# Optimization experiments

Measured on AMD Instinct MI355X. Metric: run time of the kernel, lower is better.

## Reference

```python
import jax, jax.numpy as jnp
import numpy as np

N_DOMAINS = 8
LN_EPS = 1e-5


def setup_inputs() -> dict:
    key = jax.random.key(0)
    ks = jax.random.split(key, 4)
    N, D_IN, D_HID, D_OUT = 32768, 256, 1024, 256
    x = jax.random.normal(ks[0], (N, D_IN), dtype=jnp.float32)
    domain_types = jax.random.randint(ks[1], (N,), 0, N_DOMAINS, dtype=jnp.int32)
    # Per-domain MLP parameters (8 independent experts)
    W1 = jax.random.normal(ks[2], (N_DOMAINS, D_IN, D_HID), dtype=jnp.float32) * (1.0 / np.sqrt(D_IN))
    b1 = jnp.zeros((N_DOMAINS, D_HID), dtype=jnp.float32)
    gamma = jnp.ones((N_DOMAINS, D_HID), dtype=jnp.float32)
    beta = jnp.zeros((N_DOMAINS, D_HID), dtype=jnp.float32)
    W2 = jax.random.normal(ks[3], (N_DOMAINS, D_HID, D_OUT), dtype=jnp.float32) * (1.0 / np.sqrt(D_HID))
    b2 = jnp.zeros((N_DOMAINS, D_OUT), dtype=jnp.float32)
    return {"x": x, "domain_types": domain_types, "W1": W1, "b1": b1,
            "gamma": gamma, "beta": beta, "W2": W2, "b2": b2}


def _expert_mlp(x, W1d, b1d, gd, bd, W2d, b2d):
    # Linear -> LayerNorm -> ReLU -> (Dropout: identity at eval) -> Linear
    h = x @ W1d + b1d                       # [N, hid]
    mu = jnp.mean(h, axis=-1, keepdims=True)
    var = jnp.mean(jnp.square(h - mu), axis=-1, keepdims=True)
    h = (h - mu) * jax.lax.rsqrt(var + LN_EPS) * gd + bd
    h = jax.nn.relu(h)
    return h @ W2d + b2d                    # [N, out]


def reference(x, domain_types, W1, b1, gamma, beta, W2, b2):
    # output dim == x.shape[-1] (as in the torch code: zeros(batch, x.shape[-1]))
    out = jnp.zeros((x.shape[0], x.shape[-1]), dtype=x.dtype)
    for d in range(N_DOMAINS):  # small fixed expert loop (static MoE dispatch)
        y = _expert_mlp(x, W1[d], b1[d], gamma[d], beta[d], W2[d], b2[d])
        mask = (domain_types == d)[:, None]
        out = jnp.where(mask, y, out)
    return out
```

## Files before the change

kernel.cpp:

```cpp
#include <hip/hip_runtime.h>
#include <hip/hip_bf16.h>


#define ND 8
#define NROWS 32768
#define DIN 256
#define DHID 1024
#define DOUT 256
#define MPAD 33792
#define NTILES 264

typedef short short8 __attribute__((ext_vector_type(8)));
typedef float floatx4 __attribute__((ext_vector_type(4)));

__device__ __forceinline__ unsigned short f2bf(float f) {
    unsigned u = __builtin_bit_cast(unsigned, f);
    unsigned r = u + 0x7fff + ((u >> 16) & 1);
    return (unsigned short)(r >> 16);
}
__device__ __forceinline__ float bf2f(unsigned short h) {
    unsigned u = ((unsigned)h) << 16;
    return __builtin_bit_cast(float, u);
}

#define GLDS16(gp, lp) __builtin_amdgcn_global_load_lds( \
    (const __attribute__((address_space(1))) void*)(gp), \
    (__attribute__((address_space(3))) void*)(lp), 16, 0, 0)

__global__ void transpose_both(const float* __restrict__ W1, unsigned short* __restrict__ W1T,
                               const float* __restrict__ W2, unsigned short* __restrict__ W2T,
                               int* __restrict__ cnt) {
    if (blockIdx.x == 0 && threadIdx.x < 16) cnt[threadIdx.x] = 0;
    __shared__ float t[32][33];
    int b = blockIdx.x;
    const float* in; unsigned short* out; int R, C, bx, by, z;
    if (b < 2048) {
        in = W1; out = W1T; R = DIN; C = DHID;
        bx = b & 31; by = (b >> 5) & 7; z = b >> 8;
    } else {
        b -= 2048;
        in = W2; out = W2T; R = DHID; C = DOUT;
        bx = b & 7; by = (b >> 3) & 31; z = b >> 8;
    }
    const int c0 = bx * 32, r0 = by * 32;
    const int tx = threadIdx.x & 31, ty = threadIdx.x >> 5;
    const float* src = in + (size_t)z * R * C;
    unsigned short* dst = out + (size_t)z * R * C;
#pragma unroll
    for (int i = 0; i < 32; i += 8)
        t[ty + i][tx] = src[(size_t)(r0 + ty + i) * C + c0 + tx];
    __syncthreads();
#pragma unroll
    for (int i = 0; i < 32; i += 8)
        dst[(size_t)(c0 + ty + i) * R + r0 + tx] = f2bf(t[tx][ty + i]);
}

__global__ void init_histo(const int* __restrict__ dt, int* __restrict__ perm,
                           int* __restrict__ counts) {
    const int i = blockIdx.x * 256 + threadIdx.x;
    if (i < MPAD) perm[i] = -1;
    __shared__ int lc[ND];
    if (threadIdx.x < ND) lc[threadIdx.x] = 0;
    __syncthreads();
    if (i < NROWS) atomicAdd(&lc[dt[i]], 1);
    __syncthreads();
    if (threadIdx.x < ND && lc[threadIdx.x] > 0)
        atomicAdd(&counts[threadIdx.x], lc[threadIdx.x]);
}

__global__ void make_meta(const int* __restrict__ counts, int* __restrict__ cursors,
                          int2* __restrict__ meta) {
    __shared__ int base[ND], ntc[ND];
    const int t = threadIdx.x;
    if (t == 0) {
        int off = 0;
        for (int d = 0; d < ND; d++) {
            base[d] = off;
            ntc[d] = (counts[d] + 127) >> 7;
            cursors[d] = off;
            off += ntc[d] << 7;
        }
    }
    __syncthreads();
    for (int i = t; i < NTILES; i += 64) {
        int2 m = make_int2(-1, 0);
#pragma unroll
        for (int d = 0; d < ND; d++) {
            const int ti = i - (base[d] >> 7);
            if (ti >= 0 && ti < ntc[d]) m = make_int2(d, base[d] + (ti << 7));
        }
        meta[i] = m;
    }
}

__global__ __launch_bounds__(256)
void assign_pos(const int* __restrict__ dt, int* __restrict__ cursors,
                int* __restrict__ perm, int* __restrict__ pos) {
    __shared__ int lcnt[ND];
    __shared__ int lbase[ND];
    const int tid = threadIdx.x;
    if (tid < ND) lcnt[tid] = 0;
    __syncthreads();
    const int r = blockIdx.x * 256 + tid;
    const int d = dt[r];
    const int myrank = atomicAdd(&lcnt[d], 1);
    __syncthreads();
    if (tid < ND && lcnt[tid] > 0)
        lbase[tid] = atomicAdd(&cursors[tid], lcnt[tid]);
    __syncthreads();
    const int p = lbase[d] + myrank;
    pos[r] = p;
    perm[p] = r;
}

__global__ __launch_bounds__(256)
void copy_rows(const float* __restrict__ x, const int* __restrict__ pos,
               unsigned short* __restrict__ xs) {
    const int tid = threadIdx.x;
    const int lane = tid & 63;
    const int r = blockIdx.x * 4 + (tid >> 6);
    const int p = pos[r];
    float4 v = ((const float4*)(x + (size_t)r * DIN))[lane];
    ushort4 o;
    o.x = f2bf(v.x); o.y = f2bf(v.y); o.z = f2bf(v.z); o.w = f2bf(v.w);
    ((ushort4*)(xs + (size_t)p * DIN))[lane] = o;
}

template <int K, bool ISB>
__global__ __launch_bounds__(256, 2)
void gemm_bt(const unsigned short* __restrict__ A,
             const unsigned short* __restrict__ Bt,
             const float* __restrict__ bias,
             const int2* __restrict__ meta,
             const int* __restrict__ perm,
             unsigned short* __restrict__ Cbf,
             float* __restrict__ Cf,
             const int Ntot,
             float2* __restrict__ spart,
             const float* __restrict__ gamma,
             const float* __restrict__ beta) {
    constexpr int NB = ISB ? 2 : 8;
    constexpr int NWG = NTILES * NB;
    constexpr int NS = K / 32;
    const int bid = (int)blockIdx.x;
    const int wid = (bid & 7) * (NWG >> 3) + (bid >> 3);
    const int tile = wid / NB;
    const int n0 = (wid % NB) * 128;
    const int2 md = meta[tile];
    const int dom = md.x;
    if (dom < 0) return;
    const int m0 = md.y;

    __shared__ unsigned short As[2][128 * 32];
    __shared__ unsigned short Bs[2][128 * 32];
    __shared__ float gb[ISB ? 2048 : 64];
    __shared__ float sred[2][128];

    const int tid = threadIdx.x;
    const int lane = tid & 63;
    const int w = tid >> 6;
    const int wr = w >> 1, wc = w & 1;
    const int l15 = lane & 15;

    const unsigned short* Abase = A + (size_t)m0 * K;
    const unsigned short* Bbase = Bt + (size_t)dom * Ntot * K + (size_t)n0 * K;

    if (!ISB) {
        if (tid < 128) { sred[0][tid] = 0.f; sred[1][tid] = 0.f; }
    }

    const int ma = (w * 128 + lane) >> 2;
    const int kc = lane & 3;
    float muv[2], rsv[2];
    short8 hv0{}, hv1{};
    if (ISB) {
        ((float4*)gb)[tid] = ((const float4*)(gamma + dom * DHID))[tid];
        ((float4*)(gb + 1024))[tid] = ((const float4*)(beta + dom * DHID))[tid];
#pragma unroll
        for (int h2 = 0; h2 < 2; ++h2) {
            const int rm = m0 + ma + h2 * 16;
            float s = 0.f, s2 = 0.f;
#pragma unroll
            for (int nb = 0; nb < 8; ++nb) {
                const float2 p = spart[(size_t)nb * MPAD + rm];
                s += p.x; s2 += p.y;
            }
            const float mu = s * (1.f / 1024.f);
            const float var = fmaxf(s2 * (1.f / 1024.f) - mu * mu, 0.f);
            muv[h2] = mu;
            rsv[h2] = rsqrtf(var + 1e-5f);
        }
        hv0 = *(const short8*)(Abase + (size_t)ma * K + kc * 8);
        hv1 = *(const short8*)(Abase + (size_t)(ma + 16) * K + kc * 8);
    }

#define STAGE_B(buf, t_) {                                                     \
        const int k0_ = (t_) * 32;                                             \
        _Pragma("unroll")                                                      \
        for (int it = 0; it < 2; ++it) {                                       \
            const int c = w * 128 + it * 64 + lane;                            \
            const int m_ = c >> 2, kcc = c & 3;                                \
            GLDS16(Bbase + (size_t)m_ * K + k0_ + kcc * 8,                     \
                   &Bs[buf][(w * 128 + it * 64) * 8]);                         \
        }                                                                      \
    }
#define STAGE_A_GLDS(buf, t_) {                                                \
        const int k0_ = (t_) * 32;                                             \
        _Pragma("unroll")                                                      \
        for (int it = 0; it < 2; ++it) {                                       \
            const int c = w * 128 + it * 64 + lane;                            \
            const int m_ = c >> 2, kcc = c & 3;                                \
            GLDS16(Abase + (size_t)m_ * K + k0_ + kcc * 8,                     \
                   &As[buf][(w * 128 + it * 64) * 8]);                         \
        }                                                                      \
    }
#define STAGE_A_XFRM(buf, t_) {                                                \
        const int k1 = (t_) * 32 + kc * 8;                                     \
        const float4 g0 = *(const float4*)&gb[k1];                             \
        const float4 g1 = *(const float4*)&gb[k1 + 4];                         \
        const float4 e0 = *(const float4*)&gb[1024 + k1];                      \
        const float4 e1 = *(const float4*)&gb[1024 + k1 + 4];                  \
        const float gA[8] = {g0.x, g0.y, g0.z, g0.w, g1.x, g1.y, g1.z, g1.w};  \
        const float eA[8] = {e0.x, e0.y, e0.z, e0.w, e1.x, e1.y, e1.z, e1.w};  \
        _Pragma("unroll")                                                      \
        for (int h2 = 0; h2 < 2; ++h2) {                                       \
            const float mu = muv[h2], rs = rsv[h2];                            \
            const short8 hvv = h2 ? hv1 : hv0;                                 \
            short8 o;                                                          \
            _Pragma("unroll")                                                  \
            for (int e = 0; e < 8; ++e) {                                      \
                const float rg = gA[e] * rs;                                   \
                const float v = fmaxf(fmaf(bf2f((unsigned short)hvv[e]), rg,   \
                                           fmaf(-mu, rg, eA[e])), 0.f);        \
                o[e] = (short)f2bf(v);                                         \
            }                                                                  \
            *(short8*)&As[buf][(w * 128 + h2 * 64 + lane) * 8] = o;            \
        }                                                                      \
    }
#define LOAD_H(t_) {                                                           \
        const int k0_ = (t_) * 32;                                             \
        hv0 = *(const short8*)(Abase + (size_t)ma * K + k0_ + kc * 8);         \
        hv1 = *(const short8*)(Abase + (size_t)(ma + 16) * K + k0_ + kc * 8);  \
    }

    floatx4 acc[4][4];
#pragma unroll
    for (int i = 0; i < 4; i++)
#pragma unroll
        for (int j = 0; j < 4; j++) acc[i][j] = 0.f;

    STAGE_B(0, 0)
    if (!ISB) {
        STAGE_A_GLDS(0, 0)
    } else {
        STAGE_A_XFRM(0, 0)
        LOAD_H(1)
    }
    __syncthreads();

    int cur = 0;
    const int kk = (lane >> 4) * 8;
    for (int t = 0; t < NS - 1; ++t) {
        const int nx = cur ^ 1;
        STAGE_B(nx, t + 1)
        if (!ISB) {
            STAGE_A_GLDS(nx, t + 1)
        } else {
            STAGE_A_XFRM(nx, t + 1)
            if (t + 2 < NS) LOAD_H(t + 2)
        }
        short8 a[4], b[4];
#pragma unroll
        for (int i = 0; i < 4; i++) {
            const int m = wr * 64 + i * 16 + l15;
            a[i] = *(const short8*)&As[cur][m * 32 + kk];
            const int n = wc * 64 + i * 16 + l15;
            b[i] = *(const short8*)&Bs[cur][n * 32 + kk];
        }
        __builtin_amdgcn_s_setprio(1);
#pragma unroll
        for (int i = 0; i < 4; i++)
#pragma unroll
            for (int j = 0; j < 4; j++)
                acc[i][j] = __builtin_amdgcn_mfma_f32_16x16x32_bf16(a[i], b[j], acc[i][j], 0, 0, 0);
        __builtin_amdgcn_s_setprio(0);
        __syncthreads();
        cur = nx;
    }
    {
        short8 a[4], b[4];
#pragma unroll
        for (int i = 0; i < 4; i++) {
            const int m = wr * 64 + i * 16 + l15;
            a[i] = *(const short8*)&As[cur][m * 32 + kk];
            const int n = wc * 64 + i * 16 + l15;
            b[i] = *(const short8*)&Bs[cur][n * 32 + kk];
        }
        __builtin_amdgcn_s_setprio(1);
#pragma unroll
        for (int i = 0; i < 4; i++)
#pragma unroll
            for (int j = 0; j < 4; j++)
                acc[i][j] = __builtin_amdgcn_mfma_f32_16x16x32_bf16(a[i], b[j], acc[i][j], 0, 0, 0);
        __builtin_amdgcn_s_setprio(0);
    }
#undef STAGE_B
#undef STAGE_A_GLDS
#undef STAGE_A_XFRM
#undef LOAD_H

    const int quad = lane >> 4;
    if (!ISB) {
        float bv[4];
#pragma unroll
        for (int j = 0; j < 4; j++)
            bv[j] = bias[dom * Ntot + n0 + wc * 64 + j * 16 + l15];
#pragma unroll
        for (int i = 0; i < 4; i++) {
#pragma unroll
            for (int r = 0; r < 4; r++) {
                const int rl = wr * 64 + i * 16 + quad * 4 + r;
                float s = 0.f, s2 = 0.f;
#pragma unroll
                for (int j = 0; j < 4; j++) {
                    const float v = acc[i][j][r] + bv[j];
                    Cbf[(size_t)(m0 + rl) * Ntot + n0 + wc * 64 + j * 16 + l15] = f2bf(v);
                    s += v; s2 += v * v;
                }
#pragma unroll
                for (int o = 8; o; o >>= 1) {
                    s  += __shfl_xor(s, o, 64);
                    s2 += __shfl_xor(s2, o, 64);
                }
                if (l15 == 0) {
                    atomicAdd(&sred[0][rl], s);
                    atomicAdd(&sred[1][rl], s2);
                }
            }
        }
        __syncthreads();
        if (tid < 128)
            spart[(size_t)(n0 >> 7) * MPAD + m0 + tid] =
                make_float2(sred[0][tid], sred[1][tid]);
    } else {
#pragma unroll
        for (int i = 0; i < 4; i++) {
            const int rowbase = m0 + wr * 64 + i * 16 + quad * 4;
#pragma unroll
            for (int r = 0; r < 4; r++) {
                const int orig = perm[rowbase + r];
                if (orig < 0) continue;
#pragma unroll
                for (int j = 0; j < 4; j++) {
                    const int col = n0 + wc * 64 + j * 16 + l15;
                    Cf[(size_t)orig * Ntot + col] = acc[i][j][r] + bias[dom * Ntot + col];
                }
            }
        }
    }
}

extern "C" void kernel_launch(void* const* d_in, const int* in_sizes, int n_in,
                              void* d_out, int out_size, void* d_ws, size_t ws_size,
                              hipStream_t stream) {
    const float* x = (const float*)d_in[0];
    const int* dt = (const int*)d_in[1];
    const float* W1 = (const float*)d_in[2];
    const float* b1 = (const float*)d_in[3];
    const float* gamma = (const float*)d_in[4];
    const float* beta = (const float*)d_in[5];
    const float* W2 = (const float*)d_in[6];
    const float* b2 = (const float*)d_in[7];
    float* out = (float*)d_out;

    char* ws = (char*)d_ws;
    size_t off = 0;
    auto take = [&](size_t nbytes) -> char* {
        char* p = ws + off;
        off = (off + nbytes + 255) & ~(size_t)255;
        return p;
    };
    unsigned short* W1T = (unsigned short*)take((size_t)ND * DHID * DIN * 2);
    unsigned short* W2T = (unsigned short*)take((size_t)ND * DOUT * DHID * 2);
    unsigned short* XS  = (unsigned short*)take((size_t)MPAD * DIN * 2);
    unsigned short* H   = (unsigned short*)take((size_t)MPAD * DHID * 2);
    float2* SPART = (float2*)take((size_t)8 * MPAD * 8);
    int* PERM   = (int*)take(MPAD * 4);
    int* POS    = (int*)take(NROWS * 4);
    int* CNT    = (int*)take(64);
    int2* META  = (int2*)take(NTILES * 8);
    (void)ws_size; (void)n_in; (void)in_sizes; (void)out_size;

    int* COUNTS = CNT;
    int* CURSORS = CNT + 8;

    transpose_both<<<4096, 256, 0, stream>>>(W1, W1T, W2, W2T, CNT);
    init_histo<<<MPAD / 256, 256, 0, stream>>>(dt, PERM, COUNTS);
    make_meta<<<1, 64, 0, stream>>>(COUNTS, CURSORS, META);
    assign_pos<<<NROWS / 256, 256, 0, stream>>>(dt, CURSORS, PERM, POS);
    copy_rows<<<NROWS / 4, 256, 0, stream>>>(x, POS, XS);
    gemm_bt<DIN, false><<<NTILES * 8, 256, 0, stream>>>(
        XS, W1T, b1, META, nullptr, H, nullptr, DHID, SPART, nullptr, nullptr);
    gemm_bt<DHID, true><<<NTILES * 2, 256, 0, stream>>>(
        H, W2T, b2, META, PERM, nullptr, out, DOUT, SPART, gamma, beta);
}
```

Baseline: 201.6 us.

## Split second GEMM along K into four slices with atomic output accumulation

The second GEMM (K=1024) now splits the reduction dimension into four 256-wide slices. This quadruples the number of workgroups (2112 instead of 528) to fill the GPU better, and each slice accumulates into the output with float atomics. The output is zeroed inside copy_rows. Bias is added only by the first slice, and gamma/beta staging is shrunk to the slice's range. The templated GEMM is split into two dedicated kernels. In exchange, the change adds atomic traffic on the output, recomputes the LayerNorm statistics in every slice, and makes the float summation order nondeterministic.

```diff
diff --git a/kernel.cpp b/kernel.cpp
--- a/kernel.cpp
+++ b/kernel.cpp
@@ -115,7 +115,7 @@
 
 __global__ __launch_bounds__(256)
 void copy_rows(const float* __restrict__ x, const int* __restrict__ pos,
-               unsigned short* __restrict__ xs) {
+               unsigned short* __restrict__ xs, float* __restrict__ out) {
     const int tid = threadIdx.x;
     const int lane = tid & 63;
     const int r = blockIdx.x * 4 + (tid >> 6);
@@ -124,24 +124,17 @@
     ushort4 o;
     o.x = f2bf(v.x); o.y = f2bf(v.y); o.z = f2bf(v.z); o.w = f2bf(v.w);
     ((ushort4*)(xs + (size_t)p * DIN))[lane] = o;
-}
-
-template <int K, bool ISB>
+    ((float4*)out)[(size_t)blockIdx.x * 256 + tid] = make_float4(0.f, 0.f, 0.f, 0.f);
+}
+
 __global__ __launch_bounds__(256, 2)
-void gemm_bt(const unsigned short* __restrict__ A,
-             const unsigned short* __restrict__ Bt,
-             const float* __restrict__ bias,
-             const int2* __restrict__ meta,
-             const int* __restrict__ perm,
-             unsigned short* __restrict__ Cbf,
-             float* __restrict__ Cf,
-             const int Ntot,
-             float2* __restrict__ spart,
-             const float* __restrict__ gamma,
-             const float* __restrict__ beta) {
-    constexpr int NB = ISB ? 2 : 8;
-    constexpr int NWG = NTILES * NB;
-    constexpr int NS = K / 32;
+void gemm_a(const unsigned short* __restrict__ A,
+            const unsigned short* __restrict__ Bt,
+            const float* __restrict__ bias,
+            const int2* __restrict__ meta,
+            unsigned short* __restrict__ Cbf,
+            float2* __restrict__ spart) {
+    constexpr int K = DIN, Ntot = DHID, NB = 8, NWG = NTILES * NB, NS = K / 32;
     const int bid = (int)blockIdx.x;
     const int wid = (bid & 7) * (NWG >> 3) + (bid >> 3);
     const int tile = wid / NB;
@@ -153,7 +146,6 @@
 
     __shared__ unsigned short As[2][128 * 32];
     __shared__ unsigned short Bs[2][128 * 32];
-    __shared__ float gb[ISB ? 2048 : 64];
     __shared__ float sred[2][128];
 
     const int tid = threadIdx.x;
@@ -165,36 +157,9 @@
     const unsigned short* Abase = A + (size_t)m0 * K;
     const unsigned short* Bbase = Bt + (size_t)dom * Ntot * K + (size_t)n0 * K;
 
-    if (!ISB) {
-        if (tid < 128) { sred[0][tid] = 0.f; sred[1][tid] = 0.f; }
-    }
-
-    const int ma = (w * 128 + lane) >> 2;
-    const int kc = lane & 3;
-    float muv[2], rsv[2];
-    short8 hv0{}, hv1{};
-    if (ISB) {
-        ((float4*)gb)[tid] = ((const float4*)(gamma + dom * DHID))[tid];
-        ((float4*)(gb + 1024))[tid] = ((const float4*)(beta + dom * DHID))[tid];
-#pragma unroll
-        for (int h2 = 0; h2 < 2; ++h2) {
-            const int rm = m0 + ma + h2 * 16;
-            float s = 0.f, s2 = 0.f;
-#pragma unroll
-            for (int nb = 0; nb < 8; ++nb) {
-                const float2 p = spart[(size_t)nb * MPAD + rm];
-                s += p.x; s2 += p.y;
-            }
-            const float mu = s * (1.f / 1024.f);
-            const float var = fmaxf(s2 * (1.f / 1024.f) - mu * mu, 0.f);
-            muv[h2] = mu;
-            rsv[h2] = rsqrtf(var + 1e-5f);
-        }
-        hv0 = *(const short8*)(Abase + (size_t)ma * K + kc * 8);
-        hv1 = *(const short8*)(Abase + (size_t)(ma + 16) * K + kc * 8);
-    }
-
-#define STAGE_B(buf, t_) {                                                     \
+    if (tid < 128) { sred[0][tid] = 0.f; sred[1][tid] = 0.f; }
+
+#define STAGE_AB(buf, t_) {                                                    \
         const int k0_ = (t_) * 32;                                             \
         _Pragma("unroll")                                                      \
         for (int it = 0; it < 2; ++it) {                                       \
@@ -202,24 +167,166 @@
             const int m_ = c >> 2, kcc = c & 3;                                \
             GLDS16(Bbase + (size_t)m_ * K + k0_ + kcc * 8,                     \
                    &Bs[buf][(w * 128 + it * 64) * 8]);                         \
-        }                                                                      \
-    }
-#define STAGE_A_GLDS(buf, t_) {                                                \
-        const int k0_ = (t_) * 32;                                             \
-        _Pragma("unroll")                                                      \
-        for (int it = 0; it < 2; ++it) {                                       \
-            const int c = w * 128 + it * 64 + lane;                            \
-            const int m_ = c >> 2, kcc = c & 3;                                \
             GLDS16(Abase + (size_t)m_ * K + k0_ + kcc * 8,                     \
                    &As[buf][(w * 128 + it * 64) * 8]);                         \
         }                                                                      \
     }
-#define STAGE_A_XFRM(buf, t_) {                                                \
+
+    floatx4 acc[4][4];
+#pragma unroll
+    for (int i = 0; i < 4; i++)
+#pragma unroll
+        for (int j = 0; j < 4; j++) acc[i][j] = 0.f;
+
+    STAGE_AB(0, 0)
+    __syncthreads();
+
+    int cur = 0;
+    const int kk = (lane >> 4) * 8;
+    for (int t = 0; t < NS - 1; ++t) {
+        const int nx = cur ^ 1;
+        STAGE_AB(nx, t + 1)
+        short8 a[4], b[4];
+#pragma unroll
+        for (int i = 0; i < 4; i++) {
+            const int m = wr * 64 + i * 16 + l15;
+            a[i] = *(const short8*)&As[cur][m * 32 + kk];
+            const int n = wc * 64 + i * 16 + l15;
+            b[i] = *(const short8*)&Bs[cur][n * 32 + kk];
+        }
+        __builtin_amdgcn_s_setprio(1);
+#pragma unroll
+        for (int i = 0; i < 4; i++)
+#pragma unroll
+            for (int j = 0; j < 4; j++)
+                acc[i][j] = __builtin_amdgcn_mfma_f32_16x16x32_bf16(a[i], b[j], acc[i][j], 0, 0, 0);
+        __builtin_amdgcn_s_setprio(0);
+        __syncthreads();
+        cur = nx;
+    }
+    {
+        short8 a[4], b[4];
+#pragma unroll
+        for (int i = 0; i < 4; i++) {
+            const int m = wr * 64 + i * 16 + l15;
+            a[i] = *(const short8*)&As[cur][m * 32 + kk];
+            const int n = wc * 64 + i * 16 + l15;
+            b[i] = *(const short8*)&Bs[cur][n * 32 + kk];
+        }
+        __builtin_amdgcn_s_setprio(1);
+#pragma unroll
+        for (int i = 0; i < 4; i++)
+#pragma unroll
+            for (int j = 0; j < 4; j++)
+                acc[i][j] = __builtin_amdgcn_mfma_f32_16x16x32_bf16(a[i], b[j], acc[i][j], 0, 0, 0);
+        __builtin_amdgcn_s_setprio(0);
+    }
+#undef STAGE_AB
+
+    const int quad = lane >> 4;
+    float bv[4];
+#pragma unroll
+    for (int j = 0; j < 4; j++)
+        bv[j] = bias[dom * Ntot + n0 + wc * 64 + j * 16 + l15];
+#pragma unroll
+    for (int i = 0; i < 4; i++) {
+#pragma unroll
+        for (int r = 0; r < 4; r++) {
+            const int rl = wr * 64 + i * 16 + quad * 4 + r;
+            float s = 0.f, s2 = 0.f;
+#pragma unroll
+            for (int j = 0; j < 4; j++) {
+                const float v = acc[i][j][r] + bv[j];
+                Cbf[(size_t)(m0 + rl) * Ntot + n0 + wc * 64 + j * 16 + l15] = f2bf(v);
+                s += v; s2 += v * v;
+            }
+#pragma unroll
+            for (int o = 8; o; o >>= 1) {
+                s  += __shfl_xor(s, o, 64);
+                s2 += __shfl_xor(s2, o, 64);
+            }
+            if (l15 == 0) {
+                atomicAdd(&sred[0][rl], s);
+                atomicAdd(&sred[1][rl], s2);
+            }
+        }
+    }
+    __syncthreads();
+    if (tid < 128)
+        spart[(size_t)(n0 >> 7) * MPAD + m0 + tid] =
+            make_float2(sred[0][tid], sred[1][tid]);
+}
+
+__global__ __launch_bounds__(256, 2)
+void gemm_b(const unsigned short* __restrict__ H,
+            const unsigned short* __restrict__ W2T,
+            const float* __restrict__ b2,
+            const int2* __restrict__ meta,
+            const int* __restrict__ perm,
+            float* __restrict__ out,
+            const float2* __restrict__ spart,
+            const float* __restrict__ gamma,
+            const float* __restrict__ beta) {
+    constexpr int K = DHID;
+    constexpr int NWG = NTILES * 8;
+    constexpr int NS = 8;
+    const int bid = (int)blockIdx.x;
+    const int wid = (bid & 7) * (NWG >> 3) + (bid >> 3);
+    const int tile = wid >> 3;
+    const int kq = (wid >> 1) & 3;
+    const int n0 = (wid & 1) * 128;
+    const int kbeg = kq * 256;
+    const int2 md = meta[tile];
+    const int dom = md.x;
+    if (dom < 0) return;
+    const int m0 = md.y;
+
+    __shared__ unsigned short As[2][128 * 32];
+    __shared__ unsigned short Bs[2][128 * 32];
+    __shared__ float gb[512];
+
+    const int tid = threadIdx.x;
+    const int lane = tid & 63;
+    const int w = tid >> 6;
+    const int wr = w >> 1, wc = w & 1;
+    const int l15 = lane & 15;
+
+    const unsigned short* Hbase = H + (size_t)m0 * K;
+    const unsigned short* Bbase = W2T + (size_t)dom * DOUT * K + (size_t)n0 * K;
+
+    gb[tid]       = gamma[dom * DHID + kbeg + tid];
+    gb[256 + tid] = beta[dom * DHID + kbeg + tid];
+
+    const int ma = (w * 128 + lane) >> 2;
+    const int kc = lane & 3;
+    float muv[2], rsv[2];
+#pragma unroll
+    for (int h2 = 0; h2 < 2; ++h2) {
+        const int rm = m0 + ma + h2 * 16;
+        float s = 0.f, s2 = 0.f;
+#pragma unroll
+        for (int nb = 0; nb < 8; ++nb) {
+            const float2 p = spart[(size_t)nb * MPAD + rm];
+            s += p.x; s2 += p.y;
+        }
+        const float mu = s * (1.f / 1024.f);
+        const float var = fmaxf(s2 * (1.f / 1024.f) - mu * mu, 0.f);
+        muv[h2] = mu;
+        rsv[h2] = rsqrtf(var + 1e-5f);
+    }
+    short8 hv0{}, hv1{};
+
+#define LOAD_H(t_) {                                                           \
+        const int k0_ = kbeg + (t_) * 32 + kc * 8;                             \
+        hv0 = *(const short8*)(Hbase + (size_t)ma * K + k0_);                  \
+        hv1 = *(const short8*)(Hbase + (size_t)(ma + 16) * K + k0_);           \
+    }
+#define XFRM(buf, t_) {                                                        \
         const int k1 = (t_) * 32 + kc * 8;                                     \
         const float4 g0 = *(const float4*)&gb[k1];                             \
         const float4 g1 = *(const float4*)&gb[k1 + 4];                         \
-        const float4 e0 = *(const float4*)&gb[1024 + k1];                      \
-        const float4 e1 = *(const float4*)&gb[1024 + k1 + 4];                  \
+        const float4 e0 = *(const float4*)&gb[256 + k1];                       \
+        const float4 e1 = *(const float4*)&gb[256 + k1 + 4];                   \
         const float gA[8] = {g0.x, g0.y, g0.z, g0.w, g1.x, g1.y, g1.z, g1.w};  \
         const float eA[8] = {e0.x, e0.y, e0.z, e0.w, e1.x, e1.y, e1.z, e1.w};  \
         _Pragma("unroll")                                                      \
@@ -237,10 +344,15 @@
             *(short8*)&As[buf][(w * 128 + h2 * 64 + lane) * 8] = o;            \
         }                                                                      \
     }
-#define LOAD_H(t_) {                                                           \
-        const int k0_ = (t_) * 32;                                             \
-        hv0 = *(const short8*)(Abase + (size_t)ma * K + k0_ + kc * 8);         \
-        hv1 = *(const short8*)(Abase + (size_t)(ma + 16) * K + k0_ + kc * 8);  \
+#define STAGE_B(buf, t_) {                                                     \
+        const int k0_ = kbeg + (t_) * 32;                                      \
+        _Pragma("unroll")                                                      \
+        for (int it = 0; it < 2; ++it) {                                       \
+            const int c = w * 128 + it * 64 + lane;                            \
+            const int m_ = c >> 2, kcc = c & 3;                                \
+            GLDS16(Bbase + (size_t)m_ * K + k0_ + kcc * 8,                     \
+                   &Bs[buf][(w * 128 + it * 64) * 8]);                         \
+        }                                                                      \
     }
 
     floatx4 acc[4][4];
@@ -250,12 +362,10 @@
         for (int j = 0; j < 4; j++) acc[i][j] = 0.f;
 
     STAGE_B(0, 0)
-    if (!ISB) {
-        STAGE_A_GLDS(0, 0)
-    } else {
-        STAGE_A_XFRM(0, 0)
-        LOAD_H(1)
-    }
+    LOAD_H(0)
+    __syncthreads();
+    XFRM(0, 0)
+    LOAD_H(1)
     __syncthreads();
 
     int cur = 0;
@@ -263,12 +373,8 @@
     for (int t = 0; t < NS - 1; ++t) {
         const int nx = cur ^ 1;
         STAGE_B(nx, t + 1)
-        if (!ISB) {
-            STAGE_A_GLDS(nx, t + 1)
-        } else {
-            STAGE_A_XFRM(nx, t + 1)
-            if (t + 2 < NS) LOAD_H(t + 2)
-        }
+        XFRM(nx, t + 1)
+        if (t + 2 < NS) LOAD_H(t + 2)
         short8 a[4], b[4];
 #pragma unroll
         for (int i = 0; i < 4; i++) {
@@ -304,57 +410,27 @@
                 acc[i][j] = __builtin_amdgcn_mfma_f32_16x16x32_bf16(a[i], b[j], acc[i][j], 0, 0, 0);
         __builtin_amdgcn_s_setprio(0);
     }
+#undef LOAD_H
+#undef XFRM
 #undef STAGE_B
-#undef STAGE_A_GLDS
-#undef STAGE_A_XFRM
-#undef LOAD_H
 
     const int quad = lane >> 4;
-    if (!ISB) {
-        float bv[4];
-#pragma unroll
-        for (int j = 0; j < 4; j++)
-            bv[j] = bias[dom * Ntot + n0 + wc * 64 + j * 16 + l15];
-#pragma unroll
-        for (int i = 0; i < 4; i++) {
-#pragma unroll
-            for (int r = 0; r < 4; r++) {
-                const int rl = wr * 64 + i * 16 + quad * 4 + r;
-                float s = 0.f, s2 = 0.f;
-#pragma unroll
-                for (int j = 0; j < 4; j++) {
-                    const float v = acc[i][j][r] + bv[j];
-                    Cbf[(size_t)(m0 + rl) * Ntot + n0 + wc * 64 + j * 16 + l15] = f2bf(v);
-                    s += v; s2 += v * v;
-                }
-#pragma unroll
-                for (int o = 8; o; o >>= 1) {
-                    s  += __shfl_xor(s, o, 64);
-                    s2 += __shfl_xor(s2, o, 64);
-                }
-                if (l15 == 0) {
-                    atomicAdd(&sred[0][rl], s);
-                    atomicAdd(&sred[1][rl], s2);
-                }
-            }
-        }
-        __syncthreads();
-        if (tid < 128)
-            spart[(size_t)(n0 >> 7) * MPAD + m0 + tid] =
-                make_float2(sred[0][tid], sred[1][tid]);
-    } else {
-#pragma unroll
-        for (int i = 0; i < 4; i++) {
-            const int rowbase = m0 + wr * 64 + i * 16 + quad * 4;
-#pragma unroll
-            for (int r = 0; r < 4; r++) {
-                const int orig = perm[rowbase + r];
-                if (orig < 0) continue;
-#pragma unroll
-                for (int j = 0; j < 4; j++) {
-                    const int col = n0 + wc * 64 + j * 16 + l15;
-                    Cf[(size_t)orig * Ntot + col] = acc[i][j][r] + bias[dom * Ntot + col];
-                }
+    float bv[4];
+#pragma unroll
+    for (int j = 0; j < 4; j++)
+        bv[j] = (kq == 0) ? b2[dom * DOUT + n0 + wc * 64 + j * 16 + l15] : 0.f;
+#pragma unroll
+    for (int i = 0; i < 4; i++) {
+        const int rowbase = m0 + wr * 64 + i * 16 + quad * 4;
+#pragma unroll
+        for (int r = 0; r < 4; r++) {
+            const int orig = perm[rowbase + r];
+            if (orig < 0) continue;
+#pragma unroll
+            for (int j = 0; j < 4; j++) {
+                const int col = n0 + wc * 64 + j * 16 + l15;
+                unsafeAtomicAdd(&out[(size_t)orig * DOUT + col],
+                                acc[i][j][r] + bv[j]);
             }
         }
     }
@@ -395,12 +471,11 @@
     int* CURSORS = CNT + 8;
 
     transpose_both<<<4096, 256, 0, stream>>>(W1, W1T, W2, W2T, CNT);
-    init_histo<<<MPAD / 256, 256, 0, stream>>>(dt, PERM, COUNTS);
+    init_histo<<<(MPAD + 255) / 256, 256, 0, stream>>>(dt, PERM, COUNTS);
     make_meta<<<1, 64, 0, stream>>>(COUNTS, CURSORS, META);
     assign_pos<<<NROWS / 256, 256, 0, stream>>>(dt, CURSORS, PERM, POS);
-    copy_rows<<<NROWS / 4, 256, 0, stream>>>(x, POS, XS);
-    gemm_bt<DIN, false><<<NTILES * 8, 256, 0, stream>>>(
-        XS, W1T, b1, META, nullptr, H, nullptr, DHID, SPART, nullptr, nullptr);
-    gemm_bt<DHID, true><<<NTILES * 2, 256, 0, stream>>>(
-        H, W2T, b2, META, PERM, nullptr, out, DOUT, SPART, gamma, beta);
-}
+    copy_rows<<<NROWS / 4, 256, 0, stream>>>(x, POS, XS, out);
+    gemm_a<<<NTILES * 8, 256, 0, stream>>>(XS, W1T, b1, META, H, SPART);
+    gemm_b<<<NTILES * 8, 256, 0, stream>>>(H, W2T, b2, META, PERM, out,
+                                           SPART, gamma, beta);
+}
```

After: 286.3 us. +42.0%, slower.
